# Performance work log

Hardware: AMD Instinct MI355X
Metric: run time of the kernel (lower is better)

Reference implementation:

```python
import jax, jax.numpy as jnp
import numpy as np

N = 3072      # nodes
F = 256       # nfeat
H = 8         # heads
H1 = 128      # hidden layer 1 (per head)
H2 = 128      # hidden layer 2 (per head)
OUT = 64      # out_att output dim
ALPHA = 0.2   # LeakyReLU slope
NEG = -9e15   # mask fill (as in dense GAT)


def setup_inputs() -> dict:
    key = jax.random.key(0)
    ks = jax.random.split(key, 11)
    x = jax.random.normal(ks[0], (N, F), jnp.float32)
    adj = jax.random.bernoulli(ks[1], 0.05, (N, N)).astype(jnp.float32)
    observation = jax.random.randint(ks[2], (1, N), 0, 2).astype(jnp.int32)
    s_mat = jax.random.bernoulli(ks[3], 0.05, (N, N)).astype(jnp.float32)  # unused (method='base')
    theta = jax.random.uniform(ks[4], (1, F), jnp.float32)
    W0 = jax.random.normal(ks[5], (H, F, H1), jnp.float32) * 0.05
    a0 = jax.random.normal(ks[6], (H, 2 * H1, 1), jnp.float32) * 0.05
    W1 = jax.random.normal(ks[7], (H, H1, H2), jnp.float32) * 0.05
    a1 = jax.random.normal(ks[8], (H, 2 * H2, 1), jnp.float32) * 0.05
    Wo = jax.random.normal(ks[9], (H * H2, OUT), jnp.float32) * 0.05
    ao = jax.random.normal(ks[10], (2 * OUT, 1), jnp.float32) * 0.05
    return {"x": x, "adj": adj, "observation": observation, "s_mat": s_mat,
            "theta": theta, "W0": W0, "a0": a0, "W1": W1, "a1": a1,
            "Wo": Wo, "ao": ao}


def _gat_layer(h, mask, W, a, concat):
    # Dense GAT layer: Wh = hW; e_ij = LeakyReLU(a1.Wh_i + a2.Wh_j); masked softmax; aggregate.
    Wh = h @ W                      # [N, d]
    d = W.shape[-1]
    f1 = Wh @ a[:d]                 # [N, 1]
    f2 = Wh @ a[d:]                 # [N, 1]
    e = jax.nn.leaky_relu(f1 + f2.T, ALPHA)           # [N, N]
    att = jax.nn.softmax(jnp.where(mask, e, NEG), axis=-1)
    hp = att @ Wh                   # [N, d]
    return jax.nn.elu(hp) if concat else hp


def reference(x, adj, observation, s_mat, theta, W0, a0, W1, a1, Wo, ao):
    mask = adj > 0
    # mergeState: add theta to rows of x in the seed set
    seed = (observation[0] == 1).astype(x.dtype)[:, None]   # [N, 1]
    h = x + seed * theta                                    # [N, F]
    # 8 heads, 2 stacked inner layers each (concat=True -> ELU inside)
    h0 = jax.vmap(lambda W, a: _gat_layer(h, mask, W, a, True))(W0, a0)          # [H, N, H1]
    h1 = jax.vmap(lambda hh, W, a: _gat_layer(hh, mask, W, a, True))(h0, W1, a1)  # [H, N, H2]
    hc = jnp.transpose(h1, (1, 0, 2)).reshape(N, H * H2)    # concat heads along features
    out = _gat_layer(hc, mask, Wo, ao, False)               # [N, OUT]
    return jax.nn.elu(out)
```

## Files before the change

### kernel.cpp

```cpp
#include <hip/hip_runtime.h>
#include <hip/hip_bf16.h>

#define NN 3072
#define NWORD 96
#define HH 8

typedef short short8 __attribute__((ext_vector_type(8)));
typedef float float4v __attribute__((ext_vector_type(4)));
typedef unsigned short ushort4v __attribute__((ext_vector_type(4)));

__device__ __forceinline__ float bf2f(unsigned short u) {
  union { unsigned u; float f; } v; v.u = ((unsigned)u) << 16; return v.f;
}
__device__ __forceinline__ unsigned short f2bf(float f) {
  union { float f; unsigned u; } v; v.f = f;
  unsigned r = v.u + 0x7fffu + ((v.u >> 16) & 1u);
  return (unsigned short)(r >> 16);
}
__device__ __forceinline__ float ldin(const void* p, size_t i, int isbf) {
  return isbf ? bf2f(((const unsigned short*)p)[i]) : ((const float*)p)[i];
}

__global__ __launch_bounds__(256) void k_detect(const unsigned* __restrict__ aw,
                                                int* __restrict__ flag) {
  __shared__ int s;
  if (threadIdx.x == 0) s = 0;
  __syncthreads();
  int any = 0;
  for (int i = threadIdx.x; i < 16384; i += 256)
    any |= ((aw[i] & 0xFFFFu) != 0u);
  if (any) s = 1;
  __syncthreads();
  if (threadIdx.x == 0) *flag = s;
}

__global__ __launch_bounds__(256) void k_mask(const void* __restrict__ adj,
                                              const int* __restrict__ flag,
                                              unsigned* __restrict__ maskT) {
  int isbf = *flag;
  int row = blockIdx.y;
  int j = blockIdx.x * 256 + threadIdx.x;
  bool pred = ldin(adj, (size_t)row * NN + j, isbf) != 0.f;
  unsigned long long b = __ballot(pred);
  int lane = threadIdx.x & 63;
  int word = blockIdx.x * 8 + (threadIdx.x >> 6) * 2;
  if (lane == 0) maskT[(size_t)word * NN + row] = (unsigned)b;
  else if (lane == 32) maskT[(size_t)(word + 1) * NN + row] = (unsigned)(b >> 32);
}

__global__ __launch_bounds__(256) void k_prep(const void* __restrict__ x,
                                              const int* __restrict__ obs,
                                              const void* __restrict__ theta,
                                              const void* __restrict__ W0,
                                              const void* __restrict__ W1,
                                              const void* __restrict__ Wo,
                                              const int* __restrict__ flag,
                                              unsigned short* __restrict__ h_bf,
                                              unsigned short* __restrict__ W0T,
                                              unsigned short* __restrict__ W1T,
                                              unsigned short* __restrict__ WoT) {
  __shared__ __align__(16) unsigned short tile[16][17];
  int isbf = *flag;
  int t = threadIdx.x;
  int b = blockIdx.x;
  if (b < NN) {
    int i = b * 256 + t;
    int row = i >> 8, c = i & 255;
    float v = ldin(x, i, isbf);
    if (obs[row] == 1) v += ldin(theta, c, isbf);
    h_bf[i] = f2bf(v);
    return;
  }
  b -= NN;
  const void* in; unsigned short* out; int R, C, r0, c0;
  if (b < 1024) {
    int h = b >> 7, rem = b & 127;
    in = (const char*)W0 + (size_t)h * 256 * 128 * (isbf ? 2 : 4);
    out = W0T + (size_t)h * 256 * 128;
    R = 256; C = 128; r0 = (rem >> 3) * 16; c0 = (rem & 7) * 16;
  } else if (b < 1536) {
    b -= 1024;
    int h = b >> 6, rem = b & 63;
    in = (const char*)W1 + (size_t)h * 128 * 128 * (isbf ? 2 : 4);
    out = W1T + (size_t)h * 128 * 128;
    R = 128; C = 128; r0 = (rem >> 3) * 16; c0 = (rem & 7) * 16;
  } else {
    b -= 1536;
    in = Wo; out = WoT;
    R = 1024; C = 64; r0 = (b >> 2) * 16; c0 = (b & 3) * 16;
  }
  int tc = t & 15, tr = t >> 4;
  tile[tr][tc] = f2bf(ldin(in, (size_t)(r0 + tr) * C + (c0 + tc), isbf));
  __syncthreads();
  out[(size_t)(c0 + tr) * R + (r0 + tc)] = tile[tc][tr];
}

template<int K>
__global__ __launch_bounds__(256) void k_gemm_fused(const unsigned short* __restrict__ A,
                                                    const unsigned short* __restrict__ WT,
                                                    unsigned short* __restrict__ WhTf,
                                                    long aOff, long wOff,
                                                    const void* __restrict__ avec,
                                                    const int* __restrict__ flag,
                                                    float* __restrict__ f1,
                                                    float* __restrict__ f2) {
  __shared__ __align__(16) unsigned short tile[4][2][32][17];
  __shared__ float avs[256];
  __shared__ float fp[2][8][32];
  int isbf = *flag;
  int head = blockIdx.x % HH;
  int jb = blockIdx.x / HH;
  A += (size_t)head * aOff; WT += (size_t)head * wOff;
  int rowbase = jb * 32;
  int t = threadIdx.x;
  int w = t >> 6, lane = t & 63;
  int q = lane >> 4, l = lane & 15;
  int colbase = w * 32;
  avs[t] = ldin(avec, (size_t)head * 256 + t, isbf);
  float4v acc[2][2];
#pragma unroll
  for (int rt = 0; rt < 2; rt++)
#pragma unroll
    for (int ct = 0; ct < 2; ct++) { float4v z = {0.f, 0.f, 0.f, 0.f}; acc[rt][ct] = z; }

  for (int kb = 0; kb < K; kb += 32) {
    short8 af[2], bfr[2];
#pragma unroll
    for (int rt = 0; rt < 2; rt++)
      af[rt] = *(const short8*)(A + (size_t)(rowbase + rt * 16 + l) * K + kb + q * 8);
#pragma unroll
    for (int ct = 0; ct < 2; ct++)
      bfr[ct] = *(const short8*)(WT + (size_t)(colbase + ct * 16 + l) * K + kb + q * 8);
#pragma unroll
    for (int rt = 0; rt < 2; rt++)
#pragma unroll
      for (int ct = 0; ct < 2; ct++)
        acc[rt][ct] = __builtin_amdgcn_mfma_f32_16x16x32_bf16(af[rt], bfr[ct], acc[rt][ct], 0, 0, 0);
  }
#pragma unroll
  for (int rt = 0; rt < 2; rt++)
#pragma unroll
    for (int ct = 0; ct < 2; ct++)
#pragma unroll
      for (int reg = 0; reg < 4; reg++)
        tile[w][ct][rt * 16 + q * 4 + reg][l] = f2bf(acc[rt][ct][reg]);
  __syncthreads();
#pragma unroll
  for (int ct = 0; ct < 2; ct++) {
    short8 r8;
#pragma unroll
    for (int i = 0; i < 8; i++) r8[i] = tile[w][ct][q * 8 + i][l];
    size_t chunk = ((size_t)head * (NN / 32) + jb) * 8 + (w * 2 + ct);
    *(short8*)(WhTf + chunk * 512 + lane * 8) = r8;
  }
  {
    int r = t & 31, g = t >> 5;
    int ww = g >> 1, cc = g & 1;
    float s1 = 0.f, s2 = 0.f;
#pragma unroll
    for (int li = 0; li < 16; li++) {
      float v = bf2f(tile[ww][cc][r][li]);
      s1 += v * avs[g * 16 + li];
      s2 += v * avs[128 + g * 16 + li];
    }
    fp[0][g][r] = s1; fp[1][g][r] = s2;
  }
  __syncthreads();
  if (t < 32) {
    float s1 = 0.f, s2 = 0.f;
#pragma unroll
    for (int g2 = 0; g2 < 8; g2++) { s1 += fp[0][g2][t]; s2 += fp[1][g2][t]; }
    f1[head * NN + rowbase + t] = s1;
    f2[head * NN + rowbase + t] = s2;
  }
}

template<int K, int KS>
__global__ __launch_bounds__(256) void k_gemm_out(const unsigned short* __restrict__ A,
                                                  const unsigned short* __restrict__ WT,
                                                  float* __restrict__ gpart) {
  constexpr int KC = K / KS;
  int ks = blockIdx.y;
  int rowbase = blockIdx.x * 16;
  int t = threadIdx.x;
  int w = t >> 6, lane = t & 63;
  int q = lane >> 4, l = lane & 15;
  int colbase = w * 16;
  float4v acc = {0.f, 0.f, 0.f, 0.f};
  for (int kb = ks * KC; kb < ks * KC + KC; kb += 32) {
    short8 af = *(const short8*)(A + (size_t)(rowbase + l) * K + kb + q * 8);
    short8 bfr = *(const short8*)(WT + (size_t)(colbase + l) * K + kb + q * 8);
    acc = __builtin_amdgcn_mfma_f32_16x16x32_bf16(af, bfr, acc, 0, 0, 0);
  }
#pragma unroll
  for (int reg = 0; reg < 4; reg++) {
    int r = rowbase + q * 4 + reg;
    int n = colbase + l;
    gpart[((size_t)ks * 64 + n) * NN + r] = acc[reg];
  }
}

template<int KS>
__global__ __launch_bounds__(256) void k_gemm_red(const float* __restrict__ gpart,
                                                  unsigned short* __restrict__ WhoTf) {
  int tid = blockIdx.x * 256 + threadIdx.x;
  int r = tid % NN, n = tid / NN;
  float s = 0.f;
#pragma unroll
  for (int ks = 0; ks < KS; ks++) s += gpart[((size_t)ks * 64 + n) * NN + r];
  int jb = r >> 5, q = (r >> 3) & 3, i = r & 7, ct = n >> 4, l = n & 15;
  WhoTf[((size_t)(jb * 4 + ct)) * 512 + (q * 16 + l) * 8 + i] = f2bf(s);
}

template<int DC>
__global__ __launch_bounds__(256) void k_f12f(const unsigned short* __restrict__ WhTf,
                                              const void* __restrict__ avec,
                                              const int* __restrict__ flag,
                                              float* __restrict__ f1, float* __restrict__ f2) {
  constexpr int NCT = DC / 16;
  int isbf = *flag;
  int head = blockIdx.y;
  int w = threadIdx.x >> 6, lane = threadIdx.x & 63;
  int q = lane >> 4, l = lane & 15;
  int jbIdx = blockIdx.x * 4 + w;
  size_t abase = (size_t)head * 2 * DC;
  float s1[8], s2[8];
#pragma unroll
  for (int i = 0; i < 8; i++) { s1[i] = 0.f; s2[i] = 0.f; }
#pragma unroll
  for (int ct = 0; ct < NCT; ct++) {
    short8 v = *(const short8*)(WhTf + (((size_t)head * (NN / 32) + jbIdx) * NCT + ct) * 512 + lane * 8);
    float a1v = ldin(avec, abase + ct * 16 + l, isbf);
    float a2v = ldin(avec, abase + DC + ct * 16 + l, isbf);
#pragma unroll
    for (int i = 0; i < 8; i++) {
      float f = bf2f((unsigned short)v[i]);
      s1[i] += f * a1v;
      s2[i] += f * a2v;
    }
  }
#pragma unroll
  for (int d = 1; d < 16; d <<= 1)
#pragma unroll
    for (int i = 0; i < 8; i++) {
      s1[i] += __shfl_xor(s1[i], d, 64);
      s2[i] += __shfl_xor(s2[i], d, 64);
    }
  if (l == 0) {
    int r = jbIdx * 32 + q * 8;
#pragma unroll
    for (int i = 0; i < 8; i++) {
      f1[head * NN + r + i] = s1[i];
      f2[head * NN + r + i] = s2[i];
    }
  }
}

template<int DCOL, int S>
__global__ __launch_bounds__(256, 4) void k_attn_part(
    const unsigned* __restrict__ maskT,
    const float* __restrict__ f1g, const float* __restrict__ f2g,
    const unsigned short* __restrict__ WhTf,
    unsigned short* __restrict__ pnum, float* __restrict__ pden, int NH) {
  constexpr int NCT = DCOL / 16;
  constexpr int JCH = NN / S;
  constexpr int NIT = JCH / 32;
  constexpr int CH = NCT * 512;
  constexpr int GR = CH / (256 * 8);
  __shared__ __align__(16) unsigned short Bs[2][CH];
  __shared__ __align__(16) float f2s[JCH];
  __shared__ unsigned ms[NIT * 128];

  int blk = blockIdx.x;
  int head = blk % NH;
  int rest = blk / NH;
  int js = rest % S;
  int bx = rest / S;
  int t = threadIdx.x;
  int w = t >> 6, lane = t & 63;
  int q = lane >> 4, l = lane & 15;
  int rowbase = bx * 128 + w * 32;
  int rowblk = bx * 128;
  size_t headJB = (size_t)head * (NN / 32);
  int j0 = js * JCH;

  for (int i = t; i < JCH; i += 256) f2s[i] = f2g[head * NN + j0 + i];
  for (int i = t; i < NIT * 128; i += 256)
    ms[i] = maskT[(size_t)((j0 >> 5) + (i >> 7)) * NN + rowblk + (i & 127)];
  float f1c0 = f1g[head * NN + rowbase + l] * 1.44269504f;
  float f1c1 = f1g[head * NN + rowbase + 16 + l] * 1.44269504f;

  short8 ones;
#pragma unroll
  for (int i = 0; i < 8; i++) ones[i] = (short)0x3F80;

  float4v acc[2][NCT];
#pragma unroll
  for (int rt = 0; rt < 2; rt++)
#pragma unroll
    for (int ct = 0; ct < NCT; ct++) { float4v z = {0.f, 0.f, 0.f, 0.f}; acc[rt][ct] = z; }
  float4v accd[2];
  accd[0] = float4v{0.f, 0.f, 0.f, 0.f};
  accd[1] = float4v{0.f, 0.f, 0.f, 0.f};

  short8 stg[GR];
  {
    const unsigned short* g0 = WhTf + (headJB + (j0 >> 5)) * (size_t)CH;
#pragma unroll
    for (int g = 0; g < GR; g++) stg[g] = *(const short8*)(g0 + g * 2048 + t * 8);
  }

  int cur = 0;
  for (int it = 0; it < NIT; it++) {
#pragma unroll
    for (int g = 0; g < GR; g++)
      *(short8*)(&Bs[cur][g * 2048 + t * 8]) = stg[g];
    __syncthreads();
    int itn = (it + 1 < NIT) ? it + 1 : 0;
    const unsigned short* gn = WhTf + (headJB + (j0 >> 5) + itn) * (size_t)CH;
#pragma unroll
    for (int g = 0; g < GR; g++) stg[g] = *(const short8*)(gn + g * 2048 + t * 8);

    unsigned mwc0 = ms[it * 128 + (w * 32 + l)] >> (q * 8);
    unsigned mwc1 = ms[it * 128 + (w * 32 + 16 + l)] >> (q * 8);
    float4v fac = *(const float4v*)(&f2s[it * 32 + q * 8]);
    float4v fbc = *(const float4v*)(&f2s[it * 32 + q * 8 + 4]);
    short8 bfr[NCT];
#pragma unroll
    for (int ct = 0; ct < NCT; ct++)
      bfr[ct] = *(const short8*)(&Bs[cur][ct * 512 + lane * 8]);

    float p0[8], p1[8];
#pragma unroll
    for (int i = 0; i < 8; i++) {
      float fv = (i < 4) ? fac[i] : fbc[i - 4];
      float t0 = fmaf(fv, 1.44269504f, f1c0);
      t0 = __builtin_amdgcn_fmed3f(t0, 0.2f * t0, 43.f);
      t0 = (mwc0 & (1u << i)) ? t0 : -200.f;
      p0[i] = exp2f(t0);
      float t1 = fmaf(fv, 1.44269504f, f1c1);
      t1 = __builtin_amdgcn_fmed3f(t1, 0.2f * t1, 43.f);
      t1 = (mwc1 & (1u << i)) ? t1 : -200.f;
      p1[i] = exp2f(t1);
    }
    union { __hip_bfloat162 b2[4]; short8 s8; } u0, u1;
#pragma unroll
    for (int k = 0; k < 4; k++) {
      u0.b2[k] = __float22bfloat162_rn({p0[2 * k], p0[2 * k + 1]});
      u1.b2[k] = __float22bfloat162_rn({p1[2 * k], p1[2 * k + 1]});
    }
    accd[0] = __builtin_amdgcn_mfma_f32_16x16x32_bf16(u0.s8, ones, accd[0], 0, 0, 0);
    accd[1] = __builtin_amdgcn_mfma_f32_16x16x32_bf16(u1.s8, ones, accd[1], 0, 0, 0);
#pragma unroll
    for (int ct = 0; ct < NCT; ct++) {
      acc[0][ct] = __builtin_amdgcn_mfma_f32_16x16x32_bf16(u0.s8, bfr[ct], acc[0][ct], 0, 0, 0);
      acc[1][ct] = __builtin_amdgcn_mfma_f32_16x16x32_bf16(u1.s8, bfr[ct], acc[1][ct], 0, 0, 0);
    }
    cur ^= 1;
  }

  size_t slab = (size_t)(js * NH + head);
  if (l == 0) {
#pragma unroll
    for (int rt = 0; rt < 2; rt++)
#pragma unroll
      for (int reg = 0; reg < 4; reg++)
        pden[slab * NN + rowbase + rt * 16 + q * 4 + reg] = accd[rt][reg];
  }
  int trb = rowbase >> 4;
#pragma unroll
  for (int rt = 0; rt < 2; rt++)
#pragma unroll
    for (int ct = 0; ct < NCT; ct++) {
      ushort4v u;
      u.x = f2bf(acc[rt][ct].x); u.y = f2bf(acc[rt][ct].y);
      u.z = f2bf(acc[rt][ct].z); u.w = f2bf(acc[rt][ct].w);
      size_t cidx = ((slab * (NN / 16) + trb + rt) * NCT + ct) * 256 + lane * 4;
      *(ushort4v*)(pnum + cidx) = u;
    }
}

template<int DCOL, int S>
__global__ __launch_bounds__(256) void k_attn_reduce(
    const unsigned short* __restrict__ pnum, const float* __restrict__ pden,
    void* __restrict__ outg, long outHeadOff, int outRowStride, int NH,
    const int* __restrict__ flag, int finalOut) {
  constexpr int NCT = DCOL / 16;
  int blk = blockIdx.x;
  int h = blk % NH;
  int bi = blk / NH;
  int t = threadIdx.x;
  int base = bi * 1024 + t * 4;
  int tile = base >> 8;
  int lane = (base >> 2) & 63;
  int ct = tile % NCT, tr = tile / NCT;
  int q = lane >> 4, l = lane & 15;
  int row0 = tr * 16 + q * 4;
  int col = ct * 16 + l;
  float sn[4] = {0.f, 0.f, 0.f, 0.f};
  float sd[4] = {0.f, 0.f, 0.f, 0.f};
#pragma unroll
  for (int js = 0; js < S; js++) {
    size_t sl = (size_t)(js * NH + h);
    ushort4v pv = *(const ushort4v*)(pnum + sl * (size_t)(NN * DCOL) + base);
    float4v dv = *(const float4v*)(pden + sl * NN + row0);
    sn[0] += bf2f(pv.x); sn[1] += bf2f(pv.y); sn[2] += bf2f(pv.z); sn[3] += bf2f(pv.w);
    sd[0] += dv.x; sd[1] += dv.y; sd[2] += dv.z; sd[3] += dv.w;
  }
  int f32o = finalOut && (*flag == 0);
#pragma unroll
  for (int r = 0; r < 4; r++) {
    float v = sd[r] > 0.f ? sn[r] / sd[r] : 0.f;
    v = v > 0.f ? v : expm1f(v);
    size_t idx = (size_t)h * outHeadOff + (size_t)(row0 + r) * outRowStride + col;
    if (f32o) ((float*)outg)[idx] = v;
    else ((unsigned short*)outg)[idx] = f2bf(v);
  }
}

extern "C" void kernel_launch(void* const* d_in, const int* in_sizes, int n_in,
                              void* d_out, int out_size, void* d_ws, size_t ws_size,
                              hipStream_t stream) {
  const void* x     = d_in[0];
  const void* adj   = d_in[1];
  const int*  obs   = (const int*)d_in[2];
  const void* theta = d_in[4];
  const void* W0    = d_in[5];
  const void* a0    = d_in[6];
  const void* W1    = d_in[7];
  const void* a1    = d_in[8];
  const void* Wo    = d_in[9];
  const void* ao    = d_in[10];

  char* ws = (char*)d_ws;
  size_t off = 0;
  auto alloc = [&](size_t bytes) { void* p = ws + off; off += (bytes + 255) & ~(size_t)255; return p; };
  int*            flag  = (int*)alloc(4);
  unsigned*       maskT = (unsigned*)alloc((size_t)NN * NWORD * 4);
  unsigned short* h_bf  = (unsigned short*)alloc((size_t)NN * 256 * 2);
  unsigned short* WhTf  = (unsigned short*)alloc((size_t)HH * 128 * NN * 2);
  float*          f1    = (float*)alloc((size_t)HH * NN * 4);
  float*          f2    = (float*)alloc((size_t)HH * NN * 4);
  unsigned short* h0    = (unsigned short*)alloc((size_t)HH * NN * 128 * 2);
  unsigned short* hc    = (unsigned short*)alloc((size_t)NN * 1024 * 2);
  unsigned short* W0T   = (unsigned short*)alloc((size_t)HH * 128 * 256 * 2);
  unsigned short* W1T   = (unsigned short*)alloc((size_t)HH * 128 * 128 * 2);
  unsigned short* WoT   = (unsigned short*)alloc((size_t)64 * 1024 * 2);
  unsigned short* WhoTf = (unsigned short*)alloc((size_t)64 * NN * 2);
  float*          fo1   = (float*)alloc((size_t)NN * 4);
  float*          fo2   = (float*)alloc((size_t)NN * 4);
  float*          gpart = (float*)alloc((size_t)4 * 64 * NN * 4);

  size_t fixedEnd = off;
  auto needBytes = [&](int s) {
    size_t slabs = (size_t)((s * HH > 32) ? s * HH : 32);
    return fixedEnd + (size_t)s * HH * NN * 128 * 2 + slabs * NN * 4 + 8192;
  };
  int S = (needBytes(8) <= ws_size) ? 8 : (needBytes(4) <= ws_size) ? 4 : 2;
  unsigned short* pnum = (unsigned short*)alloc((size_t)S * HH * NN * 128 * 2);
  float* pden = (float*)alloc((size_t)((S * HH > 32) ? S * HH : 32) * NN * 4);

  k_detect<<<1, 256, 0, stream>>>((const unsigned*)adj, flag);
  k_mask<<<dim3(12, NN), 256, 0, stream>>>(adj, flag, maskT);
  k_prep<<<NN + 1792, 256, 0, stream>>>(x, obs, theta, W0, W1, Wo, flag,
                                        h_bf, W0T, W1T, WoT);

  k_gemm_fused<256><<<(NN / 32) * HH, 256, 0, stream>>>(h_bf, W0T, WhTf,
                                                        0, 128 * 256, a0, flag, f1, f2);
  switch (S) {
    case 8:
      k_attn_part<128, 8><<<(NN / 128) * 8 * HH, 256, 0, stream>>>(maskT, f1, f2, WhTf, pnum, pden, HH);
      k_attn_reduce<128, 8><<<HH * NN * 128 / 1024, 256, 0, stream>>>(pnum, pden, h0, (long)NN * 128, 128, HH, flag, 0);
      break;
    case 4:
      k_attn_part<128, 4><<<(NN / 128) * 4 * HH, 256, 0, stream>>>(maskT, f1, f2, WhTf, pnum, pden, HH);
      k_attn_reduce<128, 4><<<HH * NN * 128 / 1024, 256, 0, stream>>>(pnum, pden, h0, (long)NN * 128, 128, HH, flag, 0);
      break;
    default:
      k_attn_part<128, 2><<<(NN / 128) * 2 * HH, 256, 0, stream>>>(maskT, f1, f2, WhTf, pnum, pden, HH);
      k_attn_reduce<128, 2><<<HH * NN * 128 / 1024, 256, 0, stream>>>(pnum, pden, h0, (long)NN * 128, 128, HH, flag, 0);
  }
  k_gemm_fused<128><<<(NN / 32) * HH, 256, 0, stream>>>(h0, W1T, WhTf,
                                                        (long)NN * 128, 128 * 128, a1, flag, f1, f2);
  switch (S) {
    case 8:
      k_attn_part<128, 8><<<(NN / 128) * 8 * HH, 256, 0, stream>>>(maskT, f1, f2, WhTf, pnum, pden, HH);
      k_attn_reduce<128, 8><<<HH * NN * 128 / 1024, 256, 0, stream>>>(pnum, pden, hc, 128, 1024, HH, flag, 0);
      break;
    case 4:
      k_attn_part<128, 4><<<(NN / 128) * 4 * HH, 256, 0, stream>>>(maskT, f1, f2, WhTf, pnum, pden, HH);
      k_attn_reduce<128, 4><<<HH * NN * 128 / 1024, 256, 0, stream>>>(pnum, pden, hc, 128, 1024, HH, flag, 0);
      break;
    default:
      k_attn_part<128, 2><<<(NN / 128) * 2 * HH, 256, 0, stream>>>(maskT, f1, f2, WhTf, pnum, pden, HH);
      k_attn_reduce<128, 2><<<HH * NN * 128 / 1024, 256, 0, stream>>>(pnum, pden, hc, 128, 1024, HH, flag, 0);
  }
  k_gemm_out<1024, 4><<<dim3(NN / 16, 4), 256, 0, stream>>>(hc, WoT, gpart);
  k_gemm_red<4><<<64 * NN / 256, 256, 0, stream>>>(gpart, WhoTf);
  k_f12f<64><<<dim3(NN / 128, 1), 256, 0, stream>>>(WhoTf, ao, flag, fo1, fo2);
  k_attn_part<64, 32><<<(NN / 128) * 32, 256, 0, stream>>>(maskT, fo1, fo2, WhoTf, pnum, pden, 1);
  k_attn_reduce<64, 32><<<NN * 64 / 1024, 256, 0, stream>>>(pnum, pden, d_out, 0, 64, 1, flag, 1);
}
```

Measured before the change: 300.1 us.

## Halve attention row tile to 64, fix split S=4, grid-stride mask/prep

```diff
diff --git a/kernel.cpp b/kernel.cpp
--- a/kernel.cpp
+++ b/kernel.cpp
@@ -38,14 +38,18 @@
                                               const int* __restrict__ flag,
                                               unsigned* __restrict__ maskT) {
   int isbf = *flag;
-  int row = blockIdx.y;
-  int j = blockIdx.x * 256 + threadIdx.x;
-  bool pred = ldin(adj, (size_t)row * NN + j, isbf) != 0.f;
-  unsigned long long b = __ballot(pred);
-  int lane = threadIdx.x & 63;
-  int word = blockIdx.x * 8 + (threadIdx.x >> 6) * 2;
-  if (lane == 0) maskT[(size_t)word * NN + row] = (unsigned)b;
-  else if (lane == 32) maskT[(size_t)(word + 1) * NN + row] = (unsigned)(b >> 32);
+  int t = threadIdx.x;
+  int lane = t & 63;
+  for (int chunk = blockIdx.x; chunk < NN * 12; chunk += gridDim.x) {
+    int row = chunk / 12;
+    int seg = chunk - row * 12;
+    int j = seg * 256 + t;
+    bool pred = ldin(adj, (size_t)row * NN + j, isbf) != 0.f;
+    unsigned long long b = __ballot(pred);
+    int word = seg * 8 + (t >> 6) * 2;
+    if (lane == 0) maskT[(size_t)word * NN + row] = (unsigned)b;
+    else if (lane == 32) maskT[(size_t)(word + 1) * NN + row] = (unsigned)(b >> 32);
+  }
 }
 
 __global__ __launch_bounds__(256) void k_prep(const void* __restrict__ x,
@@ -63,15 +67,16 @@
   int isbf = *flag;
   int t = threadIdx.x;
   int b = blockIdx.x;
-  if (b < NN) {
-    int i = b * 256 + t;
-    int row = i >> 8, c = i & 255;
-    float v = ldin(x, i, isbf);
-    if (obs[row] == 1) v += ldin(theta, c, isbf);
-    h_bf[i] = f2bf(v);
+  if (b < NN / 4) {
+    for (int i = b * 1024 + t; i < b * 1024 + 1024; i += 256) {
+      int row = i >> 8, c = i & 255;
+      float v = ldin(x, i, isbf);
+      if (obs[row] == 1) v += ldin(theta, c, isbf);
+      h_bf[i] = f2bf(v);
+    }
     return;
   }
-  b -= NN;
+  b -= NN / 4;
   const void* in; unsigned short* out; int R, C, r0, c0;
   if (b < 1024) {
     int h = b >> 7, rem = b & 127;
@@ -269,7 +274,7 @@
   constexpr int GR = CH / (256 * 8);
   __shared__ __align__(16) unsigned short Bs[2][CH];
   __shared__ __align__(16) float f2s[JCH];
-  __shared__ unsigned ms[NIT * 128];
+  __shared__ unsigned ms[NIT * 64];
 
   int blk = blockIdx.x;
   int head = blk % NH;
@@ -279,29 +284,24 @@
   int t = threadIdx.x;
   int w = t >> 6, lane = t & 63;
   int q = lane >> 4, l = lane & 15;
-  int rowbase = bx * 128 + w * 32;
-  int rowblk = bx * 128;
+  int rowblk = bx * 64;
+  int rowbase = rowblk + w * 16;
   size_t headJB = (size_t)head * (NN / 32);
   int j0 = js * JCH;
 
   for (int i = t; i < JCH; i += 256) f2s[i] = f2g[head * NN + j0 + i];
-  for (int i = t; i < NIT * 128; i += 256)
-    ms[i] = maskT[(size_t)((j0 >> 5) + (i >> 7)) * NN + rowblk + (i & 127)];
-  float f1c0 = f1g[head * NN + rowbase + l] * 1.44269504f;
-  float f1c1 = f1g[head * NN + rowbase + 16 + l] * 1.44269504f;
+  for (int i = t; i < NIT * 64; i += 256)
+    ms[i] = maskT[(size_t)((j0 >> 5) + (i >> 6)) * NN + rowblk + (i & 63)];
+  float f1c = f1g[head * NN + rowbase + l] * 1.44269504f;
 
   short8 ones;
 #pragma unroll
   for (int i = 0; i < 8; i++) ones[i] = (short)0x3F80;
 
-  float4v acc[2][NCT];
-#pragma unroll
-  for (int rt = 0; rt < 2; rt++)
-#pragma unroll
-    for (int ct = 0; ct < NCT; ct++) { float4v z = {0.f, 0.f, 0.f, 0.f}; acc[rt][ct] = z; }
-  float4v accd[2];
-  accd[0] = float4v{0.f, 0.f, 0.f, 0.f};
-  accd[1] = float4v{0.f, 0.f, 0.f, 0.f};
+  float4v acc[NCT];
+#pragma unroll
+  for (int ct = 0; ct < NCT; ct++) { float4v z = {0.f, 0.f, 0.f, 0.f}; acc[ct] = z; }
+  float4v accd = {0.f, 0.f, 0.f, 0.f};
 
   short8 stg[GR];
   {
@@ -321,8 +321,7 @@
 #pragma unroll
     for (int g = 0; g < GR; g++) stg[g] = *(const short8*)(gn + g * 2048 + t * 8);
 
-    unsigned mwc0 = ms[it * 128 + (w * 32 + l)] >> (q * 8);
-    unsigned mwc1 = ms[it * 128 + (w * 32 + 16 + l)] >> (q * 8);
+    unsigned mwc = ms[it * 64 + (w * 16 + l)] >> (q * 8);
     float4v fac = *(const float4v*)(&f2s[it * 32 + q * 8]);
     float4v fbc = *(const float4v*)(&f2s[it * 32 + q * 8 + 4]);
     short8 bfr[NCT];
@@ -330,54 +329,41 @@
     for (int ct = 0; ct < NCT; ct++)
       bfr[ct] = *(const short8*)(&Bs[cur][ct * 512 + lane * 8]);
 
-    float p0[8], p1[8];
+    float p[8];
 #pragma unroll
     for (int i = 0; i < 8; i++) {
       float fv = (i < 4) ? fac[i] : fbc[i - 4];
-      float t0 = fmaf(fv, 1.44269504f, f1c0);
+      float t0 = fmaf(fv, 1.44269504f, f1c);
       t0 = __builtin_amdgcn_fmed3f(t0, 0.2f * t0, 43.f);
-      t0 = (mwc0 & (1u << i)) ? t0 : -200.f;
-      p0[i] = exp2f(t0);
-      float t1 = fmaf(fv, 1.44269504f, f1c1);
-      t1 = __builtin_amdgcn_fmed3f(t1, 0.2f * t1, 43.f);
-      t1 = (mwc1 & (1u << i)) ? t1 : -200.f;
-      p1[i] = exp2f(t1);
-    }
-    union { __hip_bfloat162 b2[4]; short8 s8; } u0, u1;
-#pragma unroll
-    for (int k = 0; k < 4; k++) {
-      u0.b2[k] = __float22bfloat162_rn({p0[2 * k], p0[2 * k + 1]});
-      u1.b2[k] = __float22bfloat162_rn({p1[2 * k], p1[2 * k + 1]});
-    }
-    accd[0] = __builtin_amdgcn_mfma_f32_16x16x32_bf16(u0.s8, ones, accd[0], 0, 0, 0);
-    accd[1] = __builtin_amdgcn_mfma_f32_16x16x32_bf16(u1.s8, ones, accd[1], 0, 0, 0);
-#pragma unroll
-    for (int ct = 0; ct < NCT; ct++) {
-      acc[0][ct] = __builtin_amdgcn_mfma_f32_16x16x32_bf16(u0.s8, bfr[ct], acc[0][ct], 0, 0, 0);
-      acc[1][ct] = __builtin_amdgcn_mfma_f32_16x16x32_bf16(u1.s8, bfr[ct], acc[1][ct], 0, 0, 0);
-    }
+      t0 = (mwc & (1u << i)) ? t0 : -200.f;
+      p[i] = exp2f(t0);
+    }
+    union { __hip_bfloat162 b2[4]; short8 s8; } u0;
+#pragma unroll
+    for (int k = 0; k < 4; k++)
+      u0.b2[k] = __float22bfloat162_rn({p[2 * k], p[2 * k + 1]});
+    accd = __builtin_amdgcn_mfma_f32_16x16x32_bf16(u0.s8, ones, accd, 0, 0, 0);
+#pragma unroll
+    for (int ct = 0; ct < NCT; ct++)
+      acc[ct] = __builtin_amdgcn_mfma_f32_16x16x32_bf16(u0.s8, bfr[ct], acc[ct], 0, 0, 0);
     cur ^= 1;
   }
 
   size_t slab = (size_t)(js * NH + head);
   if (l == 0) {
 #pragma unroll
-    for (int rt = 0; rt < 2; rt++)
-#pragma unroll
-      for (int reg = 0; reg < 4; reg++)
-        pden[slab * NN + rowbase + rt * 16 + q * 4 + reg] = accd[rt][reg];
+    for (int reg = 0; reg < 4; reg++)
+      pden[slab * NN + rowbase + q * 4 + reg] = accd[reg];
   }
   int trb = rowbase >> 4;
 #pragma unroll
-  for (int rt = 0; rt < 2; rt++)
-#pragma unroll
-    for (int ct = 0; ct < NCT; ct++) {
-      ushort4v u;
-      u.x = f2bf(acc[rt][ct].x); u.y = f2bf(acc[rt][ct].y);
-      u.z = f2bf(acc[rt][ct].z); u.w = f2bf(acc[rt][ct].w);
-      size_t cidx = ((slab * (NN / 16) + trb + rt) * NCT + ct) * 256 + lane * 4;
-      *(ushort4v*)(pnum + cidx) = u;
-    }
+  for (int ct = 0; ct < NCT; ct++) {
+    ushort4v u;
+    u.x = f2bf(acc[ct].x); u.y = f2bf(acc[ct].y);
+    u.z = f2bf(acc[ct].z); u.w = f2bf(acc[ct].w);
+    size_t cidx = ((slab * (NN / 16) + trb) * NCT + ct) * 256 + lane * 4;
+    *(ushort4v*)(pnum + cidx) = u;
+  }
 }
 
 template<int DCOL, int S>
@@ -451,53 +437,25 @@
   float*          fo2   = (float*)alloc((size_t)NN * 4);
   float*          gpart = (float*)alloc((size_t)4 * 64 * NN * 4);
 
-  size_t fixedEnd = off;
-  auto needBytes = [&](int s) {
-    size_t slabs = (size_t)((s * HH > 32) ? s * HH : 32);
-    return fixedEnd + (size_t)s * HH * NN * 128 * 2 + slabs * NN * 4 + 8192;
-  };
-  int S = (needBytes(8) <= ws_size) ? 8 : (needBytes(4) <= ws_size) ? 4 : 2;
-  unsigned short* pnum = (unsigned short*)alloc((size_t)S * HH * NN * 128 * 2);
-  float* pden = (float*)alloc((size_t)((S * HH > 32) ? S * HH : 32) * NN * 4);
+  unsigned short* pnum = (unsigned short*)alloc((size_t)4 * HH * NN * 128 * 2);
+  float* pden = (float*)alloc((size_t)32 * NN * 4);
 
   k_detect<<<1, 256, 0, stream>>>((const unsigned*)adj, flag);
-  k_mask<<<dim3(12, NN), 256, 0, stream>>>(adj, flag, maskT);
-  k_prep<<<NN + 1792, 256, 0, stream>>>(x, obs, theta, W0, W1, Wo, flag,
-                                        h_bf, W0T, W1T, WoT);
+  k_mask<<<1536, 256, 0, stream>>>(adj, flag, maskT);
+  k_prep<<<NN / 4 + 1792, 256, 0, stream>>>(x, obs, theta, W0, W1, Wo, flag,
+                                            h_bf, W0T, W1T, WoT);
 
   k_gemm_fused<256><<<(NN / 32) * HH, 256, 0, stream>>>(h_bf, W0T, WhTf,
                                                         0, 128 * 256, a0, flag, f1, f2);
-  switch (S) {
-    case 8:
-      k_attn_part<128, 8><<<(NN / 128) * 8 * HH, 256, 0, stream>>>(maskT, f1, f2, WhTf, pnum, pden, HH);
-      k_attn_reduce<128, 8><<<HH * NN * 128 / 1024, 256, 0, stream>>>(pnum, pden, h0, (long)NN * 128, 128, HH, flag, 0);
-      break;
-    case 4:
-      k_attn_part<128, 4><<<(NN / 128) * 4 * HH, 256, 0, stream>>>(maskT, f1, f2, WhTf, pnum, pden, HH);
-      k_attn_reduce<128, 4><<<HH * NN * 128 / 1024, 256, 0, stream>>>(pnum, pden, h0, (long)NN * 128, 128, HH, flag, 0);
-      break;
-    default:
-      k_attn_part<128, 2><<<(NN / 128) * 2 * HH, 256, 0, stream>>>(maskT, f1, f2, WhTf, pnum, pden, HH);
-      k_attn_reduce<128, 2><<<HH * NN * 128 / 1024, 256, 0, stream>>>(pnum, pden, h0, (long)NN * 128, 128, HH, flag, 0);
-  }
+  k_attn_part<128, 4><<<(NN / 64) * 4 * HH, 256, 0, stream>>>(maskT, f1, f2, WhTf, pnum, pden, HH);
+  k_attn_reduce<128, 4><<<HH * NN * 128 / 1024, 256, 0, stream>>>(pnum, pden, h0, (long)NN * 128, 128, HH, flag, 0);
   k_gemm_fused<128><<<(NN / 32) * HH, 256, 0, stream>>>(h0, W1T, WhTf,
                                                         (long)NN * 128, 128 * 128, a1, flag, f1, f2);
-  switch (S) {
-    case 8:
-      k_attn_part<128, 8><<<(NN / 128) * 8 * HH, 256, 0, stream>>>(maskT, f1, f2, WhTf, pnum, pden, HH);
-      k_attn_reduce<128, 8><<<HH * NN * 128 / 1024, 256, 0, stream>>>(pnum, pden, hc, 128, 1024, HH, flag, 0);
-      break;
-    case 4:
-      k_attn_part<128, 4><<<(NN / 128) * 4 * HH, 256, 0, stream>>>(maskT, f1, f2, WhTf, pnum, pden, HH);
-      k_attn_reduce<128, 4><<<HH * NN * 128 / 1024, 256, 0, stream>>>(pnum, pden, hc, 128, 1024, HH, flag, 0);
-      break;
-    default:
-      k_attn_part<128, 2><<<(NN / 128) * 2 * HH, 256, 0, stream>>>(maskT, f1, f2, WhTf, pnum, pden, HH);
-      k_attn_reduce<128, 2><<<HH * NN * 128 / 1024, 256, 0, stream>>>(pnum, pden, hc, 128, 1024, HH, flag, 0);
-  }
+  k_attn_part<128, 4><<<(NN / 64) * 4 * HH, 256, 0, stream>>>(maskT, f1, f2, WhTf, pnum, pden, HH);
+  k_attn_reduce<128, 4><<<HH * NN * 128 / 1024, 256, 0, stream>>>(pnum, pden, hc, 128, 1024, HH, flag, 0);
   k_gemm_out<1024, 4><<<dim3(NN / 16, 4), 256, 0, stream>>>(hc, WoT, gpart);
   k_gemm_red<4><<<64 * NN / 256, 256, 0, stream>>>(gpart, WhoTf);
   k_f12f<64><<<dim3(NN / 128, 1), 256, 0, stream>>>(WhoTf, ao, flag, fo1, fo2);
-  k_attn_part<64, 32><<<(NN / 128) * 32, 256, 0, stream>>>(maskT, fo1, fo2, WhoTf, pnum, pden, 1);
+  k_attn_part<64, 32><<<(NN / 64) * 32, 256, 0, stream>>>(maskT, fo1, fo2, WhoTf, pnum, pden, 1);
   k_attn_reduce<64, 32><<<NN * 64 / 1024, 256, 0, stream>>>(pnum, pden, d_out, 0, 64, 1, flag, 1);
 }
```

Measured after the change: 305.4 us. No clear change (+1.8%).
